# Kernel optimization log

Measured on AMD Instinct MI355X. Metric: run time of the kernel, lower is better.

The kernel has to match this reference:

```python
import jax, jax.numpy as jnp
import numpy as np

B, T, C, HD = 4, 2048, 1024, 64

def setup_inputs() -> dict:
    key = jax.random.key(0)
    kx, kq, kk, kv = jax.random.split(key, 4)
    # Weights stored as [n_embed, head_size]; equivalent to torch Linear weight transposed.
    scale = 1.0 / np.sqrt(C)
    return {
        "x": jax.random.normal(kx, (B, T, C), dtype=jnp.float32),
        "Wq": jax.random.normal(kq, (C, HD), dtype=jnp.float32) * scale,
        "Wk": jax.random.normal(kk, (C, HD), dtype=jnp.float32) * scale,
        "Wv": jax.random.normal(kv, (C, HD), dtype=jnp.float32) * scale,
    }

def reference(x, Wq, Wk, Wv):
    # Projections (no bias)
    q = x @ Wq  # [B,T,HD]
    k = x @ Wk
    v = x @ Wv
    hd = k.shape[-1]
    # NOTE: original multiplies by sqrt(head_size) (not the usual 1/sqrt) -- faithful.
    scores = jnp.einsum("btd,bsd->bts", q, k) * (hd ** 0.5)  # [B,T,T]
    # First softmax over full (unmasked) rows
    w = jax.nn.softmax(scores, axis=-1)
    # Causal mask applied AFTER the first softmax, then a second softmax
    causal = jnp.tril(jnp.ones((q.shape[1], q.shape[1]), dtype=bool))  # [T,T]
    w = jnp.where(causal[None, :, :], w, -jnp.inf)
    w = jax.nn.softmax(w, axis=-1)
    out = jnp.einsum("bts,bsd->btd", w, v)  # [B,T,HD]
    return out
```

## Files before the change

### kernel.cpp

```cpp
#include <hip/hip_runtime.h>
#include <math.h>

#define T_  2048
#define C_  1024
#define HD_ 64

typedef __attribute__((ext_vector_type(8))) short bf16x8;
typedef __attribute__((ext_vector_type(4))) float f32x4;

#define MFMA_BF16(A, B, C) __builtin_amdgcn_mfma_f32_16x16x32_bf16(A, B, C, 0, 0, 0)

#define QSCALE 11.54156032711171f

#define EXP2F(x) __builtin_amdgcn_exp2f(x)

__device__ __forceinline__ short f2bf(float f) {
    union { float f; unsigned u; } v; v.f = f;
    unsigned r = v.u + 0x7fffu + ((v.u >> 16) & 1u);
    return (short)(r >> 16);
}
__device__ __forceinline__ float bf2f(short s) {
    union { float f; unsigned u; } v;
    v.u = ((unsigned)(unsigned short)s) << 16;
    return v.f;
}

__global__ __launch_bounds__(256) void prep_w_kernel(
    const float* __restrict__ Wq, const float* __restrict__ Wk,
    const float* __restrict__ Wv, short* __restrict__ wtf)
{
    const int m = blockIdx.y;
    const float* W = (m == 0) ? Wq : (m == 1) ? Wk : Wv;
    const int t = threadIdx.x;
    const int c = blockIdx.x * 64 + (t >> 2);
    const int hg = (t & 3) * 16;
    const int ct = m * 4 + (t & 3);
    const int c0i = c >> 6, kc = (c >> 5) & 1, lq = (c >> 3) & 3, e = c & 7;
    const float4* wp = (const float4*)(W + (size_t)c * HD_ + hg);
    #pragma unroll
    for (int u = 0; u < 4; ++u) {
        float4 f = wp[u];
        float vs[4] = {f.x, f.y, f.z, f.w};
        #pragma unroll
        for (int ei = 0; ei < 4; ++ei) {
            int h16 = u * 4 + ei;
            int L = h16 + 16 * lq;
            short hh = f2bf(vs[ei]);
            short lo = f2bf(vs[ei] - bf2f(hh));
            size_t oh = ((((size_t)(ct * 2 + 0) * 16 + c0i) * 2 + kc) * 64 + L) * 8 + e;
            size_t ol = ((((size_t)(ct * 2 + 1) * 16 + c0i) * 2 + kc) * 64 + L) * 8 + e;
            wtf[oh] = hh;
            wtf[ol] = lo;
        }
    }
}

__global__ __launch_bounds__(256) void qkv_proj_kernel(
    const float* __restrict__ x, const short* __restrict__ wtf,
    short* __restrict__ qhp, short* __restrict__ qlp,
    short* __restrict__ khp, short* __restrict__ klp,
    short* __restrict__ vtp)
{
    __shared__ __align__(16) short xh[2][16 * 64], xl[2][16 * 64];

    const int t = threadIdx.x, L = t & 63, wv = t >> 6;
    const int R0 = blockIdx.x * 16;
    const int ctq = wv;

    f32x4 acc[3];
    #pragma unroll
    for (int j = 0; j < 3; ++j) acc[j] = {0.f, 0.f, 0.f, 0.f};

    const int xrow = t >> 4, xc4 = t & 15;
    const float* xp = x + (size_t)(R0 + xrow) * C_ + xc4 * 4;
    float4 xa;
    auto loadX = [&](int c0) { xa = *(const float4*)(xp + c0); };

    const int c8 = xc4 >> 1, xhalf = xc4 & 1;
    const int slot = xrow * 64 + ((c8 ^ (xrow & 7)) * 8) + xhalf * 4;
    auto stageX = [&](int buf) {
        float vs[4] = {xa.x, xa.y, xa.z, xa.w};
        short4 vh, vl;
        short* vhp = (short*)&vh; short* vlp = (short*)&vl;
        #pragma unroll
        for (int e = 0; e < 4; ++e) {
            short hh = f2bf(vs[e]);
            vhp[e] = hh;
            vlp[e] = f2bf(vs[e] - bf2f(hh));
        }
        *(short4*)&xh[buf][slot] = vh;
        *(short4*)&xl[buf][slot] = vl;
    };

    const size_t lo8 = (size_t)L * 8;
    auto loadWF = [&](int c0i, int kc, bf16x8* w) {
        w[0] = *(const bf16x8*)(wtf + (size_t)((((ctq + 0) * 2 + 0) * 16 + c0i) * 2 + kc) * 512 + lo8);
        w[1] = *(const bf16x8*)(wtf + (size_t)((((ctq + 0) * 2 + 1) * 16 + c0i) * 2 + kc) * 512 + lo8);
        w[2] = *(const bf16x8*)(wtf + (size_t)((((ctq + 4) * 2 + 0) * 16 + c0i) * 2 + kc) * 512 + lo8);
        w[3] = *(const bf16x8*)(wtf + (size_t)((((ctq + 4) * 2 + 1) * 16 + c0i) * 2 + kc) * 512 + lo8);
        w[4] = *(const bf16x8*)(wtf + (size_t)((((ctq + 8) * 2 + 0) * 16 + c0i) * 2 + kc) * 512 + lo8);
    };

    bf16x8 wf0[5], wf1[5];
    const int arow = L & 15;

    loadX(0);
    loadWF(0, 0, wf0);
    stageX(0);
    loadX(64);
    __syncthreads();

    for (int c0i = 0; c0i < 16; ++c0i) {
        const int cur = c0i & 1;
        if (c0i < 15) {
            stageX(cur ^ 1);
            if (c0i < 14) loadX((c0i + 2) * 64);
        }
        loadWF(c0i, 1, wf1);
        {
            int ch = (L >> 4);
            int off = arow * 64 + ((ch ^ (arow & 7)) * 8);
            bf16x8 axh = *(const bf16x8*)&xh[cur][off];
            bf16x8 axl = *(const bf16x8*)&xl[cur][off];
            acc[0] = MFMA_BF16(axl, wf0[0], acc[0]);
            acc[0] = MFMA_BF16(axh, wf0[1], acc[0]);
            acc[0] = MFMA_BF16(axh, wf0[0], acc[0]);
            acc[1] = MFMA_BF16(axl, wf0[2], acc[1]);
            acc[1] = MFMA_BF16(axh, wf0[3], acc[1]);
            acc[1] = MFMA_BF16(axh, wf0[2], acc[1]);
            acc[2] = MFMA_BF16(wf0[4], axh, acc[2]);
        }
        if (c0i < 15) loadWF(c0i + 1, 0, wf0);
        {
            int ch = 4 + (L >> 4);
            int off = arow * 64 + ((ch ^ (arow & 7)) * 8);
            bf16x8 axh = *(const bf16x8*)&xh[cur][off];
            bf16x8 axl = *(const bf16x8*)&xl[cur][off];
            acc[0] = MFMA_BF16(axl, wf1[0], acc[0]);
            acc[0] = MFMA_BF16(axh, wf1[1], acc[0]);
            acc[0] = MFMA_BF16(axh, wf1[0], acc[0]);
            acc[1] = MFMA_BF16(axl, wf1[2], acc[1]);
            acc[1] = MFMA_BF16(axh, wf1[3], acc[1]);
            acc[1] = MFMA_BF16(axh, wf1[2], acc[1]);
            acc[2] = MFMA_BF16(wf1[4], axh, acc[2]);
        }
        __syncthreads();
    }

    const int quad = L >> 4;
    #pragma unroll
    for (int r = 0; r < 4; ++r) {
        int row = R0 + quad * 4 + r;
        int h = ctq * 16 + (L & 15);
        float vq = acc[0][r] * QSCALE;
        short hq = f2bf(vq);
        qhp[(size_t)row * HD_ + h] = hq;
        qlp[(size_t)row * HD_ + h] = f2bf(vq - bf2f(hq));
        float vk = acc[1][r];
        short hk = f2bf(vk);
        khp[(size_t)row * HD_ + h] = hk;
        klp[(size_t)row * HD_ + h] = f2bf(vk - bf2f(hk));
        int d = ctq * 16 + quad * 4 + r;
        int tt = R0 + (L & 15);
        int bb = tt >> 11, tl = tt & (T_ - 1);
        vtp[(size_t)(bb * 64 + d) * T_ + tl] = f2bf(acc[2][r]);
    }
}

__global__ __launch_bounds__(256) void stats_kernel(
    const short* __restrict__ qhp, const short* __restrict__ qlp,
    const short* __restrict__ khp, const short* __restrict__ klp,
    float* __restrict__ pm, float* __restrict__ sc)
{
    __shared__ float red[4 * 64 * 2];

    const int t = threadIdx.x, L = t & 63, wv = t >> 6;
    const int bt = blockIdx.x, seg = blockIdx.y, b = blockIdx.z;
    const int R0 = bt * 64, S0 = seg * 256;

    bf16x8 qfh[4][2], qfl[4][2];
    #pragma unroll
    for (int rt = 0; rt < 4; ++rt)
        #pragma unroll
        for (int dc = 0; dc < 2; ++dc) {
            int row = R0 + rt * 16 + (L & 15);
            size_t off = ((size_t)b * T_ + row) * HD_ + dc * 32 + (L >> 4) * 8;
            qfh[rt][dc] = *(const bf16x8*)(qhp + off);
            qfl[rt][dc] = *(const bf16x8*)(qlp + off);
        }

    const int colL = wv * 16 + (L & 15);
    const short* kbh = khp + ((size_t)b * T_ + S0 + colL) * HD_;
    const short* kbl = klp + ((size_t)b * T_ + S0 + colL) * HD_;
    const int cho = (L >> 4) * 8;

    bf16x8 kfh[2][2], kfl[2][2];
    auto loadK = [&](int jt, bf16x8 kh[2], bf16x8 kl[2]) {
        #pragma unroll
        for (int dc = 0; dc < 2; ++dc) {
            kh[dc] = *(const bf16x8*)(kbh + (size_t)jt * 64 * HD_ + dc * 32 + cho);
            kl[dc] = *(const bf16x8*)(kbl + (size_t)jt * 64 * HD_ + dc * 32 + cho);
        }
    };
    loadK(0, kfh[0], kfl[0]);

    f32x4 sv[4][4];
    #pragma unroll
    for (int jt = 0; jt < 4; ++jt) {
        const int cb = jt & 1;
        if (jt < 3) loadK(jt + 1, kfh[cb ^ 1], kfl[cb ^ 1]);
        const bool doStore = (S0 + jt * 64) <= (R0 + 63);
        #pragma unroll
        for (int rt = 0; rt < 4; ++rt) {
            f32x4 s = {0.f, 0.f, 0.f, 0.f};
            #pragma unroll
            for (int dc = 0; dc < 2; ++dc) {
                s = MFMA_BF16(qfl[rt][dc], kfh[cb][dc], s);
                s = MFMA_BF16(qfh[rt][dc], kfl[cb][dc], s);
                s = MFMA_BF16(qfh[rt][dc], kfh[cb][dc], s);
            }
            sv[jt][rt] = s;
            if (doStore) {
                #pragma unroll
                for (int r = 0; r < 4; ++r) {
                    int row = R0 + rt * 16 + (L >> 4) * 4 + r;
                    sc[((size_t)b * T_ + row) * T_ + S0 + jt * 64 + colL] = s[r];
                }
            }
        }
    }

    float ml[4][4], ll[4][4];
    #pragma unroll
    for (int rt = 0; rt < 4; ++rt)
        #pragma unroll
        for (int r = 0; r < 4; ++r) {
            float v0 = sv[0][rt][r], v1 = sv[1][rt][r];
            float v2 = sv[2][rt][r], v3 = sv[3][rt][r];
            float m = fmaxf(fmaxf(v0, v1), fmaxf(v2, v3));
            float l = EXP2F(v0 - m) + EXP2F(v1 - m)
                    + EXP2F(v2 - m) + EXP2F(v3 - m);
            ml[rt][r] = m; ll[rt][r] = l;
        }

    #pragma unroll
    for (int off = 1; off < 16; off <<= 1)
        #pragma unroll
        for (int rt = 0; rt < 4; ++rt)
            #pragma unroll
            for (int r = 0; r < 4; ++r) {
                float mo = __shfl_xor(ml[rt][r], off, 64);
                float lo = __shfl_xor(ll[rt][r], off, 64);
                float mn = fmaxf(ml[rt][r], mo);
                ll[rt][r] = ll[rt][r] * EXP2F(ml[rt][r] - mn) + lo * EXP2F(mo - mn);
                ml[rt][r] = mn;
            }
    if ((L & 15) == 0) {
        #pragma unroll
        for (int rt = 0; rt < 4; ++rt)
            #pragma unroll
            for (int r = 0; r < 4; ++r) {
                int row = rt * 16 + (L >> 4) * 4 + r;
                red[(wv * 64 + row) * 2 + 0] = ml[rt][r];
                red[(wv * 64 + row) * 2 + 1] = ll[rt][r];
            }
    }
    __syncthreads();
    if (t < 64) {
        float M = red[t * 2], S = red[t * 2 + 1];
        #pragma unroll
        for (int w = 1; w < 4; ++w) {
            float mo = red[(w * 64 + t) * 2], lo = red[(w * 64 + t) * 2 + 1];
            float mn = fmaxf(M, mo);
            S = S * EXP2F(M - mn) + lo * EXP2F(mo - mn);
            M = mn;
        }
        size_t o = ((size_t)((b * 32 + bt) * 8 + seg) * 64 + t) * 2;
        pm[o] = M;
        pm[o + 1] = S;
    }
}

__global__ __launch_bounds__(256) void pv_kernel(
    const float* __restrict__ sc, const short* __restrict__ vtp,
    const float* __restrict__ pm, float* __restrict__ out)
{
    __shared__ float ored[4][16][64];
    __shared__ float dred[4][16];
    __shared__ float msl[16];

    const int t = threadIdx.x, L = t & 63, wv = t >> 6;
    const int b = blockIdx.x & 3;
    const int i = blockIdx.x >> 2;
    const int p = (i < 64) ? (127 - i) : (i - 64);
    const int T0 = p * 16;

    if (t < 16) {
        int row = T0 + t;
        int bt = row >> 6, rr = row & 63;
        float M = -1e30f, S = 0.f;
        #pragma unroll
        for (int seg = 0; seg < 8; ++seg) {
            size_t o = ((size_t)((b * 32 + bt) * 8 + seg) * 64 + rr) * 2;
            float mo = pm[o], lo = pm[o + 1];
            float mn = fmaxf(M, mo);
            S = S * EXP2F(M - mn) + lo * EXP2F(mo - mn);
            M = mn;
        }
        msl[t] = M + __log2f(S);
    }
    __syncthreads();

    const int row = T0 + (L & 15);
    const float mls = msl[L & 15];
    const float* srow = sc + ((size_t)b * T_ + row) * T_;
    const short* vb = vtp + (size_t)b * 64 * T_;
    const int nJ = (T0 + 143) >> 7;
    const int cq = (L >> 4) * 8;

    f32x4 ov[4];
    #pragma unroll
    for (int dt = 0; dt < 4; ++dt) ov[dt] = {0.f, 0.f, 0.f, 0.f};
    float dn = 0.f;

    float4 sa0, sa1, sb0, sb1;
    bf16x8 va0, va1, va2, va3, vb0, vb1, vb2, vb3;

#define LDS_(jt, s0, s1) { int c0_ = (jt) * 128 + wv * 32 + cq;                  \
        s0 = *(const float4*)(srow + c0_); s1 = *(const float4*)(srow + c0_ + 4); }
#define LDV_(jt, v0, v1, v2, v3) { int c0_ = (jt) * 128 + wv * 32 + cq;          \
        v0 = *(const bf16x8*)(vb + (size_t)( 0 + (L & 15)) * T_ + c0_);          \
        v1 = *(const bf16x8*)(vb + (size_t)(16 + (L & 15)) * T_ + c0_);          \
        v2 = *(const bf16x8*)(vb + (size_t)(32 + (L & 15)) * T_ + c0_);          \
        v3 = *(const bf16x8*)(vb + (size_t)(48 + (L & 15)) * T_ + c0_); }
#define BODY_(jt, s0, s1, v0, v1, v2, v3) {                                      \
        const int c0_ = (jt) * 128 + wv * 32 + cq;                               \
        float vs_[8] = {s0.x, s0.y, s0.z, s0.w, s1.x, s1.y, s1.z, s1.w};         \
        bf16x8 ef_;                                                              \
        _Pragma("unroll")                                                        \
        for (int e = 0; e < 8; ++e) {                                            \
            float pvv = EXP2F(vs_[e] - mls);                                     \
            float evv = (c0_ + e <= row) ? __expf(pvv) : 0.f;                    \
            dn += evv;                                                           \
            ef_[e] = f2bf(evv);                                                  \
        }                                                                        \
        ov[0] = MFMA_BF16(ef_, v0, ov[0]);                                       \
        ov[1] = MFMA_BF16(ef_, v1, ov[1]);                                       \
        ov[2] = MFMA_BF16(ef_, v2, ov[2]);                                       \
        ov[3] = MFMA_BF16(ef_, v3, ov[3]); }

    LDS_(0, sa0, sa1)
    LDV_(0, va0, va1, va2, va3)
    int jt = 0;
    for (; jt + 2 <= nJ; jt += 2) {
        LDS_(jt + 1, sb0, sb1)
        LDV_(jt + 1, vb0, vb1, vb2, vb3)
        BODY_(jt, sa0, sa1, va0, va1, va2, va3)
        if (jt + 2 < nJ) {
            LDS_(jt + 2, sa0, sa1)
            LDV_(jt + 2, va0, va1, va2, va3)
        }
        BODY_(jt + 1, sb0, sb1, vb0, vb1, vb2, vb3)
    }
    if (jt < nJ) {
        BODY_(jt, sa0, sa1, va0, va1, va2, va3)
    }
#undef LDS_
#undef LDV_
#undef BODY_

    dn += __shfl_xor(dn, 16, 64);
    dn += __shfl_xor(dn, 32, 64);
    if (L < 16) dred[wv][L] = dn;
    #pragma unroll
    for (int dt = 0; dt < 4; ++dt)
        #pragma unroll
        for (int r = 0; r < 4; ++r)
            ored[wv][(L >> 4) * 4 + r][dt * 16 + (L & 15)] = ov[dt][r];
    __syncthreads();

    const int orow = t >> 4, d0 = (t & 15) * 4;
    float D = dred[0][orow] + dred[1][orow] + dred[2][orow] + dred[3][orow];
    float di = 1.f / D;
    float4 o;
    o.x = (ored[0][orow][d0 + 0] + ored[1][orow][d0 + 0]
         + ored[2][orow][d0 + 0] + ored[3][orow][d0 + 0]) * di;
    o.y = (ored[0][orow][d0 + 1] + ored[1][orow][d0 + 1]
         + ored[2][orow][d0 + 1] + ored[3][orow][d0 + 1]) * di;
    o.z = (ored[0][orow][d0 + 2] + ored[1][orow][d0 + 2]
         + ored[2][orow][d0 + 2] + ored[3][orow][d0 + 2]) * di;
    o.w = (ored[0][orow][d0 + 3] + ored[1][orow][d0 + 3]
         + ored[2][orow][d0 + 3] + ored[3][orow][d0 + 3]) * di;
    *(float4*)(out + ((size_t)b * T_ + T0 + orow) * HD_ + d0) = o;
}

extern "C" void kernel_launch(void* const* d_in, const int* in_sizes, int n_in,
                              void* d_out, int out_size, void* d_ws, size_t ws_size,
                              hipStream_t stream) {
    (void)in_sizes; (void)n_in; (void)out_size; (void)ws_size;
    const float* x  = (const float*)d_in[0];
    const float* Wq = (const float*)d_in[1];
    const float* Wk = (const float*)d_in[2];
    const float* Wv = (const float*)d_in[3];
    float* outp = (float*)d_out;

    char* ws = (char*)d_ws;
    short* wt  = (short*)ws;
    float* pm  = (float*)ws;
    short* qh = (short*)(ws + 786432);
    short* ql = (short*)(ws + 786432 + 1048576);
    short* kh = (short*)(ws + 786432 + 2 * 1048576);
    short* kl = (short*)(ws + 786432 + 3 * 1048576);
    short* vt = (short*)(ws + 786432 + 4 * 1048576);
    float* sc = (float*)(ws + 8388608);

    prep_w_kernel<<<dim3(16, 3), 256, 0, stream>>>(Wq, Wk, Wv, wt);
    qkv_proj_kernel<<<dim3(512), 256, 0, stream>>>(x, wt, qh, ql, kh, kl, vt);
    stats_kernel<<<dim3(32, 8, 4), 256, 0, stream>>>(qh, ql, kh, kl, pm, sc);
    pv_kernel<<<dim3(512), 256, 0, stream>>>(sc, vt, pm, outp);
}
```

Before: 135.5 us.

## Fuse score/stats kernel into PV kernel, computing row stats per 16-row block

Merges the stats kernel and the PV kernel into one launch. Each block now computes full-row scores for its own 16 rows over all 2048 keys, with waves splitting the key range, and merges the online max/sum in LDS before the PV phase. This removes a kernel launch and the partial-stats buffer round trip. The cost is that each block holds only one Q row tile, so K data is re-read by 128 blocks per batch instead of 32, and the amount of score MFMA work per block varies less favourably.

```diff
diff --git a/kernel.cpp b/kernel.cpp
--- a/kernel.cpp
+++ b/kernel.cpp
@@ -167,142 +167,110 @@
     }
 }
 
-__global__ __launch_bounds__(256) void stats_kernel(
+__global__ __launch_bounds__(256) void fused_attn_kernel(
     const short* __restrict__ qhp, const short* __restrict__ qlp,
     const short* __restrict__ khp, const short* __restrict__ klp,
-    float* __restrict__ pm, float* __restrict__ sc)
+    const short* __restrict__ vtp, float* __restrict__ sc,
+    float* __restrict__ out)
 {
-    __shared__ float red[4 * 64 * 2];
-
-    const int t = threadIdx.x, L = t & 63, wv = t >> 6;
-    const int bt = blockIdx.x, seg = blockIdx.y, b = blockIdx.z;
-    const int R0 = bt * 64, S0 = seg * 256;
-
-    bf16x8 qfh[4][2], qfl[4][2];
-    #pragma unroll
-    for (int rt = 0; rt < 4; ++rt)
-        #pragma unroll
-        for (int dc = 0; dc < 2; ++dc) {
-            int row = R0 + rt * 16 + (L & 15);
-            size_t off = ((size_t)b * T_ + row) * HD_ + dc * 32 + (L >> 4) * 8;
-            qfh[rt][dc] = *(const bf16x8*)(qhp + off);
-            qfl[rt][dc] = *(const bf16x8*)(qlp + off);
-        }
-
-    const int colL = wv * 16 + (L & 15);
-    const short* kbh = khp + ((size_t)b * T_ + S0 + colL) * HD_;
-    const short* kbl = klp + ((size_t)b * T_ + S0 + colL) * HD_;
-    const int cho = (L >> 4) * 8;
-
-    bf16x8 kfh[2][2], kfl[2][2];
-    auto loadK = [&](int jt, bf16x8 kh[2], bf16x8 kl[2]) {
-        #pragma unroll
-        for (int dc = 0; dc < 2; ++dc) {
-            kh[dc] = *(const bf16x8*)(kbh + (size_t)jt * 64 * HD_ + dc * 32 + cho);
-            kl[dc] = *(const bf16x8*)(kbl + (size_t)jt * 64 * HD_ + dc * 32 + cho);
-        }
-    };
-    loadK(0, kfh[0], kfl[0]);
-
-    f32x4 sv[4][4];
-    #pragma unroll
-    for (int jt = 0; jt < 4; ++jt) {
-        const int cb = jt & 1;
-        if (jt < 3) loadK(jt + 1, kfh[cb ^ 1], kfl[cb ^ 1]);
-        const bool doStore = (S0 + jt * 64) <= (R0 + 63);
-        #pragma unroll
-        for (int rt = 0; rt < 4; ++rt) {
-            f32x4 s = {0.f, 0.f, 0.f, 0.f};
-            #pragma unroll
-            for (int dc = 0; dc < 2; ++dc) {
-                s = MFMA_BF16(qfl[rt][dc], kfh[cb][dc], s);
-                s = MFMA_BF16(qfh[rt][dc], kfl[cb][dc], s);
-                s = MFMA_BF16(qfh[rt][dc], kfh[cb][dc], s);
-            }
-            sv[jt][rt] = s;
-            if (doStore) {
-                #pragma unroll
-                for (int r = 0; r < 4; ++r) {
-                    int row = R0 + rt * 16 + (L >> 4) * 4 + r;
-                    sc[((size_t)b * T_ + row) * T_ + S0 + jt * 64 + colL] = s[r];
-                }
-            }
-        }
-    }
-
-    float ml[4][4], ll[4][4];
-    #pragma unroll
-    for (int rt = 0; rt < 4; ++rt)
-        #pragma unroll
-        for (int r = 0; r < 4; ++r) {
-            float v0 = sv[0][rt][r], v1 = sv[1][rt][r];
-            float v2 = sv[2][rt][r], v3 = sv[3][rt][r];
-            float m = fmaxf(fmaxf(v0, v1), fmaxf(v2, v3));
-            float l = EXP2F(v0 - m) + EXP2F(v1 - m)
-                    + EXP2F(v2 - m) + EXP2F(v3 - m);
-            ml[rt][r] = m; ll[rt][r] = l;
-        }
-
-    #pragma unroll
-    for (int off = 1; off < 16; off <<= 1)
-        #pragma unroll
-        for (int rt = 0; rt < 4; ++rt)
-            #pragma unroll
-            for (int r = 0; r < 4; ++r) {
-                float mo = __shfl_xor(ml[rt][r], off, 64);
-                float lo = __shfl_xor(ll[rt][r], off, 64);
-                float mn = fmaxf(ml[rt][r], mo);
-                ll[rt][r] = ll[rt][r] * EXP2F(ml[rt][r] - mn) + lo * EXP2F(mo - mn);
-                ml[rt][r] = mn;
-            }
-    if ((L & 15) == 0) {
-        #pragma unroll
-        for (int rt = 0; rt < 4; ++rt)
-            #pragma unroll
-            for (int r = 0; r < 4; ++r) {
-                int row = rt * 16 + (L >> 4) * 4 + r;
-                red[(wv * 64 + row) * 2 + 0] = ml[rt][r];
-                red[(wv * 64 + row) * 2 + 1] = ll[rt][r];
-            }
-    }
-    __syncthreads();
-    if (t < 64) {
-        float M = red[t * 2], S = red[t * 2 + 1];
-        #pragma unroll
-        for (int w = 1; w < 4; ++w) {
-            float mo = red[(w * 64 + t) * 2], lo = red[(w * 64 + t) * 2 + 1];
-            float mn = fmaxf(M, mo);
-            S = S * EXP2F(M - mn) + lo * EXP2F(mo - mn);
-            M = mn;
-        }
-        size_t o = ((size_t)((b * 32 + bt) * 8 + seg) * 64 + t) * 2;
-        pm[o] = M;
-        pm[o + 1] = S;
-    }
-}
-
-__global__ __launch_bounds__(256) void pv_kernel(
-    const float* __restrict__ sc, const short* __restrict__ vtp,
-    const float* __restrict__ pm, float* __restrict__ out)
-{
+    __shared__ float red[4][16][2];
+    __shared__ float msl[16];
     __shared__ float ored[4][16][64];
     __shared__ float dred[4][16];
-    __shared__ float msl[16];
 
     const int t = threadIdx.x, L = t & 63, wv = t >> 6;
-    const int b = blockIdx.x & 3;
-    const int i = blockIdx.x >> 2;
-    const int p = (i < 64) ? (127 - i) : (i - 64);
+    const int k = blockIdx.x >> 1, half = blockIdx.x & 1;
+    const int b = k >> 6, j = k & 63;
+    const int p = half ? (127 - j) : j;
     const int T0 = p * 16;
 
+    {
+        const int cho = (L >> 4) * 8;
+        bf16x8 qfh[2], qfl[2];
+        #pragma unroll
+        for (int dc = 0; dc < 2; ++dc) {
+            int row = T0 + (L & 15);
+            size_t off = ((size_t)b * T_ + row) * HD_ + dc * 32 + cho;
+            qfh[dc] = *(const bf16x8*)(qhp + off);
+            qfl[dc] = *(const bf16x8*)(qlp + off);
+        }
+
+        const int colbase = wv * 512 + (L & 15);
+        const short* kbh = khp + ((size_t)b * T_ + colbase) * HD_ + cho;
+        const short* kbl = klp + ((size_t)b * T_ + colbase) * HD_ + cho;
+
+        bf16x8 kfh[2][2], kfl[2][2];
+        auto loadK = [&](int ct, bf16x8 kh[2], bf16x8 kl[2]) {
+            #pragma unroll
+            for (int dc = 0; dc < 2; ++dc) {
+                kh[dc] = *(const bf16x8*)(kbh + (size_t)ct * 16 * HD_ + dc * 32);
+                kl[dc] = *(const bf16x8*)(kbl + (size_t)ct * 16 * HD_ + dc * 32);
+            }
+        };
+        loadK(0, kfh[0], kfl[0]);
+
+        float ml[4], ll[4];
+        #pragma unroll
+        for (int r = 0; r < 4; ++r) { ml[r] = -1e30f; ll[r] = 0.f; }
+
+        for (int bq = 0; bq < 8; ++bq) {
+            f32x4 sv[4];
+            #pragma unroll
+            for (int jj = 0; jj < 4; ++jj) {
+                const int ct = bq * 4 + jj;
+                const int cb = ct & 1;
+                if (ct < 31) loadK(ct + 1, kfh[cb ^ 1], kfl[cb ^ 1]);
+                f32x4 s = {0.f, 0.f, 0.f, 0.f};
+                #pragma unroll
+                for (int dc = 0; dc < 2; ++dc) {
+                    s = MFMA_BF16(qfl[dc], kfh[cb][dc], s);
+                    s = MFMA_BF16(qfh[dc], kfl[cb][dc], s);
+                    s = MFMA_BF16(qfh[dc], kfh[cb][dc], s);
+                }
+                sv[jj] = s;
+                if (wv * 512 + ct * 16 <= T0 + 15) {
+                    #pragma unroll
+                    for (int r = 0; r < 4; ++r) {
+                        int row = T0 + (L >> 4) * 4 + r;
+                        sc[((size_t)b * T_ + row) * T_ + colbase + ct * 16] = s[r];
+                    }
+                }
+            }
+            #pragma unroll
+            for (int r = 0; r < 4; ++r) {
+                float v0 = sv[0][r], v1 = sv[1][r], v2 = sv[2][r], v3 = sv[3][r];
+                float mb = fmaxf(fmaxf(v0, v1), fmaxf(v2, v3));
+                float lb = EXP2F(v0 - mb) + EXP2F(v1 - mb)
+                         + EXP2F(v2 - mb) + EXP2F(v3 - mb);
+                float mn = fmaxf(ml[r], mb);
+                ll[r] = ll[r] * EXP2F(ml[r] - mn) + lb * EXP2F(mb - mn);
+                ml[r] = mn;
+            }
+        }
+        #pragma unroll
+        for (int off = 1; off < 16; off <<= 1)
+            #pragma unroll
+            for (int r = 0; r < 4; ++r) {
+                float mo = __shfl_xor(ml[r], off, 64);
+                float lo = __shfl_xor(ll[r], off, 64);
+                float mn = fmaxf(ml[r], mo);
+                ll[r] = ll[r] * EXP2F(ml[r] - mn) + lo * EXP2F(mo - mn);
+                ml[r] = mn;
+            }
+        if ((L & 15) == 0) {
+            #pragma unroll
+            for (int r = 0; r < 4; ++r) {
+                red[wv][(L >> 4) * 4 + r][0] = ml[r];
+                red[wv][(L >> 4) * 4 + r][1] = ll[r];
+            }
+        }
+    }
+    __syncthreads();
     if (t < 16) {
-        int row = T0 + t;
-        int bt = row >> 6, rr = row & 63;
-        float M = -1e30f, S = 0.f;
-        #pragma unroll
-        for (int seg = 0; seg < 8; ++seg) {
-            size_t o = ((size_t)((b * 32 + bt) * 8 + seg) * 64 + rr) * 2;
-            float mo = pm[o], lo = pm[o + 1];
+        float M = red[0][t][0], S = red[0][t][1];
+        #pragma unroll
+        for (int w = 1; w < 4; ++w) {
+            float mo = red[w][t][0], lo = red[w][t][1];
             float mn = fmaxf(M, mo);
             S = S * EXP2F(M - mn) + lo * EXP2F(mo - mn);
             M = mn;
@@ -406,7 +374,6 @@
 
     char* ws = (char*)d_ws;
     short* wt  = (short*)ws;
-    float* pm  = (float*)ws;
     short* qh = (short*)(ws + 786432);
     short* ql = (short*)(ws + 786432 + 1048576);
     short* kh = (short*)(ws + 786432 + 2 * 1048576);
@@ -416,6 +383,5 @@
 
     prep_w_kernel<<<dim3(16, 3), 256, 0, stream>>>(Wq, Wk, Wv, wt);
     qkv_proj_kernel<<<dim3(512), 256, 0, stream>>>(x, wt, qh, ql, kh, kl, vt);
-    stats_kernel<<<dim3(32, 8, 4), 256, 0, stream>>>(qh, ql, kh, kl, pm, sc);
-    pv_kernel<<<dim3(512), 256, 0, stream>>>(sc, vt, pm, outp);
-}
+    fused_attn_kernel<<<dim3(512), 256, 0, stream>>>(qh, ql, kh, kl, vt, sc, outp);
+}
```

Result: slower. 144.2 us (+6.4%).
